# Optimization experiments

Measured on AMD Instinct MI355X. Metric: run time of the kernel, lower is better.

The kernel has to match this reference:

```python
import jax, jax.numpy as jnp
import numpy as np

C = 1024          # channels
H = 8             # num_channels (heads)
D = C // H        # channel_dim
POS = 16          # pos_dim (hard-coded in module)
MAX_FREQ = 16.0
MIN_FREQ = 1.0
HALF_S = 16       # samples_per_dim=32 -> offsets -16..16 -> S=33
S = 2 * HALF_S + 1


def setup_inputs() -> dict:
    key = jax.random.key(0)
    ks = jax.random.split(key, 8)
    B, L = 2, 2048
    s = 0.02  # realistic small init scale for learned weights
    return {
        "x": jax.random.normal(ks[0], (B, L, C), jnp.float32),
        "w_wave": jax.random.normal(ks[1], (3 * H, C), jnp.float32) * s,
        "b_wave": jnp.zeros((3 * H,), jnp.float32),
        "w_query": jax.random.normal(ks[2], (H * POS, C), jnp.float32) * s,
        "b_query": jnp.zeros((H * POS,), jnp.float32),
        "w_key": jax.random.normal(ks[3], (POS,), jnp.float32) * s,  # key_proj: Linear(1, POS, bias=False)
        "w_out": jax.random.normal(ks[4], (C, C), jnp.float32) * s,
        "w_se1": jax.random.normal(ks[5], (C // 4, C), jnp.float32) * s,
        "b_se1": jnp.zeros((C // 4,), jnp.float32),
        "w_se2": jax.random.normal(ks[6], (C, C // 4), jnp.float32) * s,
        "b_se2": jnp.zeros((C,), jnp.float32),
    }


def reference(x, w_wave, b_wave, w_query, b_query, w_key, w_out, w_se1, b_se1, w_se2, b_se2):
    B, L, Cc = x.shape
    offsets = jnp.arange(-HALF_S, HALF_S + 1, dtype=jnp.float32)  # stride_grid[:, 0], (S,)

    # wave params -> per-token, per-head freq / phase / decay
    wp = jax.nn.silu(x @ w_wave.T + b_wave).reshape(B, L, 3, H).transpose(0, 1, 3, 2)  # (B,L,H,3)
    freq = jax.nn.sigmoid(wp[..., 0]) * (MAX_FREQ - MIN_FREQ) + MIN_FREQ  # (B,L,H)
    phase = jnp.tanh(wp[..., 1]) * MAX_FREQ                               # (B,L,H)
    decay = jax.nn.sigmoid(wp[..., 2]) * 9.5 + 0.5                        # (B,L,H)
    freq_avg = freq.mean(axis=2)   # (B,L)
    phase_avg = phase.mean(axis=2) # (B,L)

    # learned fractional sample positions along the sequence
    centers = jnp.arange(L, dtype=jnp.float32)
    sample_pos = (centers[None, :, None]
                  + offsets[None, None, :] * freq_avg[..., None]
                  + phase_avg[..., None])                                 # (B,L,S)
    valid = (sample_pos >= 0) & (sample_pos < L)                          # (B,L,S)
    idx = jnp.clip(sample_pos.astype(jnp.int32), 0, L - 1)

    # dynamic gather of values at computed indices: (B,L,S,C)
    values = jax.vmap(lambda xf, i: xf[i])(x, idx)
    values = values.reshape(B, L, S, H, D).transpose(0, 1, 3, 2, 4)       # (B,L,H,S,D)

    queries = jax.nn.silu(x @ w_query.T + b_query).reshape(B, L, H, POS)  # (B,L,H,POS)
    rel_dist = jnp.abs(jnp.abs(offsets)[None, None, None, :] * freq[..., None])  # (B,L,H,S)
    keys = rel_dist[..., None] * w_key                                    # (B,L,H,S,POS)

    logits = jnp.einsum('blhd,blhsd->blhs', queries, keys) * (POS ** -0.5)
    vmask = valid[:, :, None, :]                                          # (B,L,1,S) -> broadcast (B,L,H,S)
    logits = jnp.where(vmask, logits, -jnp.inf)
    envelope = jnp.exp(-rel_dist / jnp.clip(decay[..., None], 0.1, None))

    attn = jax.nn.softmax(logits, axis=-1) * envelope * vmask
    attn = attn / (attn.sum(axis=-1, keepdims=True) + 1e-8)

    out = jnp.einsum('blhsd,blhs->blhd', values, attn).reshape(B, L, Cc)

    # SE-style channel gating
    se = jax.nn.sigmoid(jax.nn.silu(out @ w_se1.T + b_se1) @ w_se2.T + b_se2)
    out = (out * se) @ w_out.T                                            # (B,L,C) (spatial=(L,))

    entropy = -(attn * jnp.log(attn + 1e-8)).sum(axis=-1).mean()
    return out, -entropy
```

## Files before the change

kernel.cpp:

```cpp
#include <hip/hip_runtime.h>

typedef unsigned short u16;
typedef unsigned int u32;
typedef __attribute__((ext_vector_type(8))) __bf16 bf16x8;
typedef __attribute__((ext_vector_type(4))) float f32x4;

#define L_SEQ 2048
#define NROWS 4096
#define NHEAD 8
#define SWIN 33

__device__ __forceinline__ u16 f2b(float f) {
  u32 u = __float_as_uint(f);
  u += 0x7fffu + ((u >> 16) & 1u);
  return (u16)(u >> 16);
}
__device__ __forceinline__ float b2f(u32 lo16) { return __uint_as_float(lo16 << 16); }

__device__ __forceinline__ float sigmoidf_(float x) { return 1.f / (1.f + expf(-x)); }
__device__ __forceinline__ float siluf_(float x) { return x / (1.f + expf(-x)); }

__device__ __forceinline__ void gload_lds16(void* g, void* l) {
  __builtin_amdgcn_global_load_lds((__attribute__((address_space(1))) void*)g,
                                   (__attribute__((address_space(3))) void*)l, 16, 0, 0);
}

#define RPB 4
__global__ __launch_bounds__(256) void wave_params_kernel(
    const float* __restrict__ x, const float* __restrict__ w_wave,
    const float* __restrict__ b_wave, float* __restrict__ params,
    u16* __restrict__ xb,
    const float* __restrict__ wq, const float* __restrict__ w1,
    const float* __restrict__ w2, const float* __restrict__ wo,
    u16* __restrict__ wqb, u16* __restrict__ w1b, u16* __restrict__ w2b,
    u16* __restrict__ wob) {
  __shared__ float xs[RPB][1024];
  __shared__ float wp[RPB][24];
  const int t = threadIdx.x;
  const int bx = blockIdx.x;
  if (bx >= 1024) {
    size_t i = (size_t)(bx - 1024) * 256 + t;
    const float* src;
    u16* dst;
    if (i < 32768) { src = wq; dst = wqb; }
    else if ((i -= 32768) < 65536) { src = w1; dst = w1b; }
    else if ((i -= 65536) < 65536) { src = w2; dst = w2b; }
    else if ((i -= 65536) < 262144) { src = wo; dst = wob; }
    else return;
    const float4 v = *(const float4*)(src + i * 4);
    uint2 pk;
    pk.x = (u32)f2b(v.x) | ((u32)f2b(v.y) << 16);
    pk.y = (u32)f2b(v.z) | ((u32)f2b(v.w) << 16);
    *(uint2*)(dst + i * 4) = pk;
    return;
  }
  const int row0 = bx * RPB;
  const float4* xv = (const float4*)(x + (size_t)row0 * 1024);
  float4* xsv = (float4*)&xs[0][0];
  uint2* xbv = (uint2*)(xb + (size_t)row0 * 1024);
#pragma unroll
  for (int i = 0; i < RPB; ++i) {
    const float4 v = xv[t + 256 * i];
    xsv[t + 256 * i] = v;
    uint2 pk;
    pk.x = (u32)f2b(v.x) | ((u32)f2b(v.y) << 16);
    pk.y = (u32)f2b(v.z) | ((u32)f2b(v.w) << 16);
    xbv[t + 256 * i] = pk;
  }
  __syncthreads();
  const int wv = t >> 6, lane = t & 63;
#pragma unroll
  for (int oi = 0; oi < 6; ++oi) {
    const int o = wv * 6 + oi;
    float w[16];
#pragma unroll
    for (int k = 0; k < 16; ++k) w[k] = w_wave[o * 1024 + lane + 64 * k];
    const float bo = b_wave[o];
    float d[RPB];
#pragma unroll
    for (int r = 0; r < RPB; ++r) {
      d[r] = 0.f;
#pragma unroll
      for (int k = 0; k < 16; ++k) d[r] += w[k] * xs[r][lane + 64 * k];
    }
#pragma unroll
    for (int r = 0; r < RPB; ++r) {
#pragma unroll
      for (int off = 32; off; off >>= 1) d[r] += __shfl_xor(d[r], off);
    }
    if (lane == 0) {
#pragma unroll
      for (int r = 0; r < RPB; ++r) wp[r][o] = siluf_(d[r] + bo);
    }
  }
  __syncthreads();
  if (t < RPB * 8) {
    const int r = t >> 3, h = t & 7;
    float* pr = params + (size_t)(row0 + r) * 18;
    pr[h] = sigmoidf_(wp[r][h]) * 15.f + 1.f;
    pr[8 + h] = sigmoidf_(wp[r][16 + h]) * 9.5f + 0.5f;
  }
  if (t < RPB) {
    float fs = 0.f, ps = 0.f;
    for (int h = 0; h < 8; ++h) {
      fs += sigmoidf_(wp[t][h]);
      ps += tanhf(wp[t][8 + h]);
    }
    float* pr = params + (size_t)(row0 + t) * 18;
    pr[16] = fs * (15.f / 8.f) + 1.f;
    pr[17] = ps * (16.f / 8.f);
  }
}

template <int MODE, int TM, int TN, int BK, int ENT = 0>
__global__ __launch_bounds__(256) void gemm_bt(
    const u16* __restrict__ A, const u16* __restrict__ Bw,
    const float* __restrict__ bias, const u16* __restrict__ aux,
    const float* __restrict__ wkey, const float* __restrict__ entpart,
    float* __restrict__ entslot, void* __restrict__ outp, int N, int K) {
  __shared__ __align__(16) u16 As[2 * TM * BK];
  __shared__ __align__(16) u16 Bs[2 * TN * BK];
  const int t = threadIdx.x;
  const int bm = blockIdx.x, bn = blockIdx.y;
  if (ENT && bn == (int)gridDim.y - 1) {
    if (bm != 0) return;
    __shared__ float ws2[4];
    float s = 0.f;
#pragma unroll
    for (int i = 0; i < 16; ++i) s += entpart[t + 256 * i];
#pragma unroll
    for (int o = 32; o; o >>= 1) s += __shfl_xor(s, o);
    if ((t & 63) == 0) ws2[t >> 6] = s;
    __syncthreads();
    if (t == 0) *entslot = ws2[0] + ws2[1] + ws2[2] + ws2[3];
    return;
  }
  constexpr int TPR = BK / 8;
  constexpr int RPP = 256 / TPR;
  const int rowS = t / TPR;
  const int colX = ((t & (TPR - 1)) ^ (rowS & (TPR - 1))) * 8;
  const u16* Ag = A + (size_t)(bm * TM + rowS) * K + colX;
  const u16* Bg = Bw + (size_t)(bn * TN + rowS) * K + colX;
  constexpr int NI = TM / 32, NJ = TN / 32;
  f32x4 acc[NI][NJ] = {};
  const int lane = t & 63, wv = t >> 6;
  const int wm = (wv >> 1) * (TM / 2);
  const int wn = (wv & 1) * (TN / 2);
  const int frow = lane & 15, quad = lane >> 4;
  auto stage = [&](int buf, int kt) {
    char* Ab = (char*)As + buf * (TM * BK * 2);
    char* Bb = (char*)Bs + buf * (TN * BK * 2);
#pragma unroll
    for (int r = 0; r < TM; r += RPP)
      gload_lds16((void*)(Ag + kt + (size_t)r * K), Ab + r * BK * 2 + t * 16);
#pragma unroll
    for (int r = 0; r < TN; r += RPP)
      gload_lds16((void*)(Bg + kt + (size_t)r * K), Bb + r * BK * 2 + t * 16);
  };
  stage(0, 0);
  int pb = 0;
  for (int kt = 0; kt < K; kt += BK, pb ^= 1) {
    __syncthreads();
    if (kt + BK < K) stage(pb ^ 1, kt + BK);
#pragma unroll
    for (int kk = 0; kk < BK; kk += 32) {
      bf16x8 af[NI], bfr[NJ];
#pragma unroll
      for (int i = 0; i < NI; ++i) {
        const int rr = wm + i * 16 + frow;
        af[i] = *(bf16x8*)&As[pb * TM * BK + rr * BK + ((((kk >> 3) + quad) ^ (rr & (TPR - 1))) * 8)];
      }
#pragma unroll
      for (int j = 0; j < NJ; ++j) {
        const int rr = wn + j * 16 + frow;
        bfr[j] = *(bf16x8*)&Bs[pb * TN * BK + rr * BK + ((((kk >> 3) + quad) ^ (rr & (TPR - 1))) * 8)];
      }
#pragma unroll
      for (int i = 0; i < NI; ++i)
#pragma unroll
        for (int j = 0; j < NJ; ++j)
          acc[i][j] = __builtin_amdgcn_mfma_f32_16x16x32_bf16(af[i], bfr[j], acc[i][j], 0, 0, 0);
    }
  }
  if (MODE == 4) {
    const float bq = bias[bn * TN + wn + frow];
    const float wkf = wkey[frow];
    const int h = bn * 2 + (wn >> 4);
#pragma unroll
    for (int i = 0; i < NI; ++i)
#pragma unroll
      for (int r = 0; r < 4; ++r) {
        float w = siluf_(acc[i][0][r] + bq) * wkf;
        w += __shfl_xor(w, 1); w += __shfl_xor(w, 2);
        w += __shfl_xor(w, 4); w += __shfl_xor(w, 8);
        if (frow == 0) {
          const int gm = bm * TM + wm + i * 16 + quad * 4 + r;
          ((float*)outp)[gm * 8 + h] = w;
        }
      }
    return;
  }
#pragma unroll
  for (int i = 0; i < NI; ++i)
#pragma unroll
    for (int j = 0; j < NJ; ++j)
#pragma unroll
      for (int r = 0; r < 4; ++r) {
        const int gm = bm * TM + wm + i * 16 + quad * 4 + r;
        const int gn = bn * TN + wn + j * 16 + frow;
        float v = acc[i][j][r];
        const size_t o = (size_t)gm * N + gn;
        if (MODE == 0) { v = siluf_(v + bias[gn]); ((float*)outp)[o] = v; }
        if (MODE == 1) { v = siluf_(v + bias[gn]); ((u16*)outp)[o] = f2b(v); }
        if (MODE == 2) { v = sigmoidf_(v + bias[gn]) * b2f(aux[o]); ((u16*)outp)[o] = f2b(v); }
        if (MODE == 3) { ((float*)outp)[o] = v; }
      }
}

__global__ __launch_bounds__(256, 2) void attn_kernel(
    const u16* __restrict__ xb, const float* __restrict__ params,
    const float* __restrict__ qkbuf, u16* __restrict__ outb,
    float* __restrict__ entpart) {
  __shared__ float pf[18];
  __shared__ float qkL[8];
  __shared__ int idxL[SWIN];
  __shared__ int validL[SWIN];
  __shared__ float attnL[NHEAD][SWIN];
  __shared__ float entW[4];
  const int t = threadIdx.x;
  const int bx = blockIdx.x;
  const int row = ((bx & 7) << 9) | (bx >> 3);
  const int b = row >> 11, l = row & 2047;
  if (t < 18) pf[t] = params[(size_t)row * 18 + t];
  if (t >= 64 && t < 72) qkL[t - 64] = qkbuf[(size_t)row * 8 + (t - 64)] * 0.25f;
  __syncthreads();
  if (t < SWIN) {
    const float pos = (float)l + (float)(t - 16) * pf[16] + pf[17];
    validL[t] = (pos >= 0.f) && (pos < (float)L_SEQ);
    int id = (int)pos;
    idxL[t] = min(max(id, 0), L_SEQ - 1);
  }
  __syncthreads();
  const int wv = t >> 6, lane = t & 63;
  float entacc = 0.f;
#pragma unroll
  for (int it = 0; it < 2; ++it) {
    const int h = wv + 4 * it;
    const bool act = lane < SWIN;
    const int s = act ? lane : 0;
    const float rel = fabsf((float)(s - 16)) * pf[h];
    const float logit = rel * qkL[h];
    const bool vs = act && validL[s];
    float m = vs ? logit : -INFINITY;
#pragma unroll
    for (int o = 32; o; o >>= 1) m = fmaxf(m, __shfl_xor(m, o));
    float p = vs ? expf(logit - m) : 0.f;
    float sm = p;
#pragma unroll
    for (int o = 32; o; o >>= 1) sm += __shfl_xor(sm, o);
    const float soft = sm > 0.f ? p / sm : 0.f;
    const float env = expf(-rel / fmaxf(pf[8 + h], 0.1f));
    float a = soft * env;
    float as = a;
#pragma unroll
    for (int o = 32; o; o >>= 1) as += __shfl_xor(as, o);
    a = a / (as + 1e-8f);
    if (act) attnL[h][s] = a;
    float et = a * logf(a + 1e-8f);
#pragma unroll
    for (int o = 32; o; o >>= 1) et += __shfl_xor(et, o);
    entacc += et;
  }
  if (lane == 0) entW[wv] = entacc;
  __syncthreads();
  if (t == 0) entpart[bx] = (entW[0] + entW[1] + entW[2] + entW[3]) * (1.f / 32768.f);
  const u16* xbase = xb + (size_t)b * L_SEQ * 1024 + 4 * t;
  const int h = t >> 5;
  float4 acc = make_float4(0.f, 0.f, 0.f, 0.f);
  uint2 v0[17], v1[16];
#pragma unroll
  for (int k = 0; k < 17; ++k) v0[k] = *(const uint2*)(xbase + (size_t)idxL[k] * 1024);
  __builtin_amdgcn_sched_barrier(0);
#pragma unroll
  for (int k = 0; k < 16; ++k) v1[k] = *(const uint2*)(xbase + (size_t)idxL[17 + k] * 1024);
  __builtin_amdgcn_sched_barrier(0);
#pragma unroll
  for (int k = 0; k < 17; ++k) {
    const float a_ = attnL[h][k];
    acc.x += a_ * b2f(v0[k].x & 0xffffu);
    acc.y += a_ * b2f(v0[k].x >> 16);
    acc.z += a_ * b2f(v0[k].y & 0xffffu);
    acc.w += a_ * b2f(v0[k].y >> 16);
  }
  __builtin_amdgcn_sched_barrier(0);
#pragma unroll
  for (int k = 0; k < 16; ++k) {
    const float a_ = attnL[h][17 + k];
    acc.x += a_ * b2f(v1[k].x & 0xffffu);
    acc.y += a_ * b2f(v1[k].x >> 16);
    acc.z += a_ * b2f(v1[k].y & 0xffffu);
    acc.w += a_ * b2f(v1[k].y >> 16);
  }
  const size_t o4 = (size_t)row * 1024 + 4 * t;
  uint2 pk;
  pk.x = (u32)f2b(acc.x) | ((u32)f2b(acc.y) << 16);
  pk.y = (u32)f2b(acc.z) | ((u32)f2b(acc.w) << 16);
  *(uint2*)(outb + o4) = pk;
}

extern "C" void kernel_launch(void* const* d_in, const int* in_sizes, int n_in,
                              void* d_out, int out_size, void* d_ws, size_t ws_size,
                              hipStream_t stream) {
  const float* x = (const float*)d_in[0];
  const float* w_wave = (const float*)d_in[1];
  const float* b_wave = (const float*)d_in[2];
  const float* w_query = (const float*)d_in[3];
  const float* b_query = (const float*)d_in[4];
  const float* w_key = (const float*)d_in[5];
  const float* w_out = (const float*)d_in[6];
  const float* w_se1 = (const float*)d_in[7];
  const float* b_se1 = (const float*)d_in[8];
  const float* w_se2 = (const float*)d_in[9];
  const float* b_se2 = (const float*)d_in[10];
  float* out = (float*)d_out;
  char* ws = (char*)d_ws;
  size_t off = 0;
  auto alloc = [&](size_t bytes) { void* p = ws + off; off += (bytes + 255) & ~(size_t)255; return p; };
  float* params = (float*)alloc(NROWS * 18 * 4);
  float* qkbuf = (float*)alloc((size_t)NROWS * 8 * 4);
  float* entpart = (float*)alloc(NROWS * 4);
  u16* outb = (u16*)alloc((size_t)NROWS * 1024 * 2);
  u16* t1b = (u16*)alloc((size_t)NROWS * 256 * 2);
  u16* gb = (u16*)alloc((size_t)NROWS * 1024 * 2);
  u16* xb = (u16*)alloc((size_t)NROWS * 1024 * 2);
  u16* wqb = (u16*)alloc(128 * 1024 * 2);
  u16* w1b = (u16*)alloc(256 * 1024 * 2);
  u16* w2b = (u16*)alloc(1024 * 256 * 2);
  u16* wob = (u16*)alloc((size_t)1024 * 1024 * 2);
  float* entslot = out + (out_size - 1);

  wave_params_kernel<<<dim3(1024 + 1664), 256, 0, stream>>>(
      x, w_wave, b_wave, params, xb, w_query, w_se1, w_se2, w_out, wqb, w1b, w2b, wob);
  gemm_bt<4, 64, 32, 64><<<dim3(64, 4), 256, 0, stream>>>(
      xb, wqb, b_query, nullptr, w_key, nullptr, nullptr, qkbuf, 128, 1024);
  attn_kernel<<<dim3(NROWS), 256, 0, stream>>>(xb, params, qkbuf, outb, entpart);
  gemm_bt<1, 64, 32, 64, 1><<<dim3(64, 9), 256, 0, stream>>>(
      outb, w1b, b_se1, nullptr, nullptr, entpart, entslot, t1b, 256, 1024);
  gemm_bt<2, 128, 64, 64><<<dim3(32, 16), 256, 0, stream>>>(
      t1b, w2b, b_se2, outb, nullptr, nullptr, nullptr, gb, 1024, 256);
  gemm_bt<3, 128, 64, 64><<<dim3(32, 16), 256, 0, stream>>>(
      gb, wob, nullptr, nullptr, nullptr, nullptr, nullptr, out, 1024, 1024);
}
```

Before: 182.2 us.

## Fuse query projection GEMM into prologue kernel and enlarge SE/output GEMM tiles

The query-projection GEMM now runs inside the first kernel as 256 extra blocks. It reads fp32 x and w_query directly and converts them to bf16 in registers on the way into LDS. This removes one kernel launch and the separate w_query bf16 conversion, and lets that GEMM overlap with the wave-param and weight-conversion blocks. Separately, the SE1, SE2 and output GEMMs use wider N tiles (64 and 128), which halves their grid sizes and raises per-block reuse. The cost is fewer blocks to fill the CUs and more LDS per block in the fused kernel.

Result: slower. 188.9 us (+3.7%).

```diff
diff --git a/kernel.cpp b/kernel.cpp
--- a/kernel.cpp
+++ b/kernel.cpp
@@ -25,36 +25,108 @@
                                    (__attribute__((address_space(3))) void*)l, 16, 0, 0);
 }
 
+__device__ __forceinline__ uint2 pk2(float a, float b, float c, float d) {
+  uint2 p;
+  p.x = (u32)f2b(a) | ((u32)f2b(b) << 16);
+  p.y = (u32)f2b(c) | ((u32)f2b(d) << 16);
+  return p;
+}
+
 #define RPB 4
-__global__ __launch_bounds__(256) void wave_params_kernel(
+__global__ __launch_bounds__(256) void mega_kernel(
     const float* __restrict__ x, const float* __restrict__ w_wave,
     const float* __restrict__ b_wave, float* __restrict__ params,
     u16* __restrict__ xb,
-    const float* __restrict__ wq, const float* __restrict__ w1,
-    const float* __restrict__ w2, const float* __restrict__ wo,
-    u16* __restrict__ wqb, u16* __restrict__ w1b, u16* __restrict__ w2b,
-    u16* __restrict__ wob) {
+    const float* __restrict__ wq, const float* __restrict__ b_query,
+    const float* __restrict__ wkey, float* __restrict__ qkbuf,
+    const float* __restrict__ w1, const float* __restrict__ w2,
+    const float* __restrict__ wo,
+    u16* __restrict__ w1b, u16* __restrict__ w2b, u16* __restrict__ wob) {
   __shared__ float xs[RPB][1024];
   __shared__ float wp[RPB][24];
+  __shared__ __align__(16) u16 qkA[2][64 * 64];
+  __shared__ __align__(16) u16 qkB[2][32 * 64];
   const int t = threadIdx.x;
   const int bx = blockIdx.x;
-  if (bx >= 1024) {
-    size_t i = (size_t)(bx - 1024) * 256 + t;
+  const int lane = t & 63, wv = t >> 6;
+
+  if (bx < 256) {
+    const int bm = bx >> 2, bn = bx & 3;
+    const int rA = t >> 2, jA = t & 3;
+    const int rB = t >> 3, jB = t & 7;
+    const float* ag = x + (size_t)(bm * 64 + rA) * 1024 + 16 * jA;
+    const float* bg = wq + (size_t)(bn * 32 + rB) * 1024 + 8 * jB;
+    const int wm = (wv >> 1) * 32, wn = (wv & 1) * 16;
+    const int frow = lane & 15, quad = lane >> 4;
+    f32x4 acc[2] = {};
+    float4 a4[4], b4[2];
+    auto loadregs = [&](int kt) {
+#pragma unroll
+      for (int q = 0; q < 4; ++q) a4[q] = *(const float4*)(ag + kt + 4 * q);
+#pragma unroll
+      for (int q = 0; q < 2; ++q) b4[q] = *(const float4*)(bg + kt + 4 * q);
+    };
+    loadregs(0);
+    int pb = 0;
+    for (int kt = 0; kt < 1024; kt += 64, pb ^= 1) {
+      uint2 pa0 = pk2(a4[0].x, a4[0].y, a4[0].z, a4[0].w);
+      uint2 pa1 = pk2(a4[1].x, a4[1].y, a4[1].z, a4[1].w);
+      uint2 pa2 = pk2(a4[2].x, a4[2].y, a4[2].z, a4[2].w);
+      uint2 pa3 = pk2(a4[3].x, a4[3].y, a4[3].z, a4[3].w);
+      uint2 pb0 = pk2(b4[0].x, b4[0].y, b4[0].z, b4[0].w);
+      uint2 pb1 = pk2(b4[1].x, b4[1].y, b4[1].z, b4[1].w);
+      const int cA0 = (2 * jA) ^ (rA & 7), cA1 = (2 * jA + 1) ^ (rA & 7);
+      *(uint4*)&qkA[pb][rA * 64 + cA0 * 8] = make_uint4(pa0.x, pa0.y, pa1.x, pa1.y);
+      *(uint4*)&qkA[pb][rA * 64 + cA1 * 8] = make_uint4(pa2.x, pa2.y, pa3.x, pa3.y);
+      const int cB = jB ^ (rB & 7);
+      *(uint4*)&qkB[pb][rB * 64 + cB * 8] = make_uint4(pb0.x, pb0.y, pb1.x, pb1.y);
+      if (kt + 64 < 1024) loadregs(kt + 64);
+      __syncthreads();
+#pragma unroll
+      for (int kk = 0; kk < 64; kk += 32) {
+        bf16x8 af[2], bfr;
+#pragma unroll
+        for (int i = 0; i < 2; ++i) {
+          const int rr = wm + i * 16 + frow;
+          af[i] = *(bf16x8*)&qkA[pb][rr * 64 + ((((kk >> 3) + quad) ^ (rr & 7)) * 8)];
+        }
+        const int rn = wn + frow;
+        bfr = *(bf16x8*)&qkB[pb][rn * 64 + ((((kk >> 3) + quad) ^ (rn & 7)) * 8)];
+#pragma unroll
+        for (int i = 0; i < 2; ++i)
+          acc[i] = __builtin_amdgcn_mfma_f32_16x16x32_bf16(af[i], bfr, acc[i], 0, 0, 0);
+      }
+    }
+    const float bq = b_query[bn * 32 + wn + frow];
+    const float wkf = wkey[frow];
+    const int h = bn * 2 + (wv & 1);
+#pragma unroll
+    for (int i = 0; i < 2; ++i)
+#pragma unroll
+      for (int r = 0; r < 4; ++r) {
+        float w = siluf_(acc[i][r] + bq) * wkf;
+        w += __shfl_xor(w, 1); w += __shfl_xor(w, 2);
+        w += __shfl_xor(w, 4); w += __shfl_xor(w, 8);
+        if (frow == 0) {
+          const int gm = bm * 64 + wm + i * 16 + quad * 4 + r;
+          qkbuf[gm * 8 + h] = w;
+        }
+      }
+    return;
+  }
+  if (bx >= 1280) {
+    size_t i = (size_t)(bx - 1280) * 256 + t;
     const float* src;
     u16* dst;
-    if (i < 32768) { src = wq; dst = wqb; }
-    else if ((i -= 32768) < 65536) { src = w1; dst = w1b; }
+    if (i < 65536) { src = w1; dst = w1b; }
     else if ((i -= 65536) < 65536) { src = w2; dst = w2b; }
     else if ((i -= 65536) < 262144) { src = wo; dst = wob; }
     else return;
     const float4 v = *(const float4*)(src + i * 4);
-    uint2 pk;
-    pk.x = (u32)f2b(v.x) | ((u32)f2b(v.y) << 16);
-    pk.y = (u32)f2b(v.z) | ((u32)f2b(v.w) << 16);
-    *(uint2*)(dst + i * 4) = pk;
+    *(uint2*)(dst + i * 4) = pk2(v.x, v.y, v.z, v.w);
     return;
   }
-  const int row0 = bx * RPB;
+  const int row0 = (bx - 256) * RPB;
   const float4* xv = (const float4*)(x + (size_t)row0 * 1024);
   float4* xsv = (float4*)&xs[0][0];
   uint2* xbv = (uint2*)(xb + (size_t)row0 * 1024);
@@ -62,13 +134,9 @@
   for (int i = 0; i < RPB; ++i) {
     const float4 v = xv[t + 256 * i];
     xsv[t + 256 * i] = v;
-    uint2 pk;
-    pk.x = (u32)f2b(v.x) | ((u32)f2b(v.y) << 16);
-    pk.y = (u32)f2b(v.z) | ((u32)f2b(v.w) << 16);
-    xbv[t + 256 * i] = pk;
-  }
-  __syncthreads();
-  const int wv = t >> 6, lane = t & 63;
+    xbv[t + 256 * i] = pk2(v.x, v.y, v.z, v.w);
+  }
+  __syncthreads();
 #pragma unroll
   for (int oi = 0; oi < 6; ++oi) {
     const int o = wv * 6 + oi;
@@ -116,8 +184,8 @@
 __global__ __launch_bounds__(256) void gemm_bt(
     const u16* __restrict__ A, const u16* __restrict__ Bw,
     const float* __restrict__ bias, const u16* __restrict__ aux,
-    const float* __restrict__ wkey, const float* __restrict__ entpart,
-    float* __restrict__ entslot, void* __restrict__ outp, int N, int K) {
+    const float* __restrict__ entpart, float* __restrict__ entslot,
+    void* __restrict__ outp, int N, int K) {
   __shared__ __align__(16) u16 As[2 * TM * BK];
   __shared__ __align__(16) u16 Bs[2 * TN * BK];
   const int t = threadIdx.x;
@@ -182,24 +250,6 @@
           acc[i][j] = __builtin_amdgcn_mfma_f32_16x16x32_bf16(af[i], bfr[j], acc[i][j], 0, 0, 0);
     }
   }
-  if (MODE == 4) {
-    const float bq = bias[bn * TN + wn + frow];
-    const float wkf = wkey[frow];
-    const int h = bn * 2 + (wn >> 4);
-#pragma unroll
-    for (int i = 0; i < NI; ++i)
-#pragma unroll
-      for (int r = 0; r < 4; ++r) {
-        float w = siluf_(acc[i][0][r] + bq) * wkf;
-        w += __shfl_xor(w, 1); w += __shfl_xor(w, 2);
-        w += __shfl_xor(w, 4); w += __shfl_xor(w, 8);
-        if (frow == 0) {
-          const int gm = bm * TM + wm + i * 16 + quad * 4 + r;
-          ((float*)outp)[gm * 8 + h] = w;
-        }
-      }
-    return;
-  }
 #pragma unroll
   for (int i = 0; i < NI; ++i)
 #pragma unroll
@@ -210,7 +260,6 @@
         const int gn = bn * TN + wn + j * 16 + frow;
         float v = acc[i][j][r];
         const size_t o = (size_t)gm * N + gn;
-        if (MODE == 0) { v = siluf_(v + bias[gn]); ((float*)outp)[o] = v; }
         if (MODE == 1) { v = siluf_(v + bias[gn]); ((u16*)outp)[o] = f2b(v); }
         if (MODE == 2) { v = sigmoidf_(v + bias[gn]) * b2f(aux[o]); ((u16*)outp)[o] = f2b(v); }
         if (MODE == 3) { ((float*)outp)[o] = v; }
@@ -302,10 +351,7 @@
     acc.w += a_ * b2f(v1[k].y >> 16);
   }
   const size_t o4 = (size_t)row * 1024 + 4 * t;
-  uint2 pk;
-  pk.x = (u32)f2b(acc.x) | ((u32)f2b(acc.y) << 16);
-  pk.y = (u32)f2b(acc.z) | ((u32)f2b(acc.w) << 16);
-  *(uint2*)(outb + o4) = pk;
+  *(uint2*)(outb + o4) = pk2(acc.x, acc.y, acc.z, acc.w);
 }
 
 extern "C" void kernel_launch(void* const* d_in, const int* in_sizes, int n_in,
@@ -333,21 +379,19 @@
   u16* t1b = (u16*)alloc((size_t)NROWS * 256 * 2);
   u16* gb = (u16*)alloc((size_t)NROWS * 1024 * 2);
   u16* xb = (u16*)alloc((size_t)NROWS * 1024 * 2);
-  u16* wqb = (u16*)alloc(128 * 1024 * 2);
   u16* w1b = (u16*)alloc(256 * 1024 * 2);
   u16* w2b = (u16*)alloc(1024 * 256 * 2);
   u16* wob = (u16*)alloc((size_t)1024 * 1024 * 2);
   float* entslot = out + (out_size - 1);
 
-  wave_params_kernel<<<dim3(1024 + 1664), 256, 0, stream>>>(
-      x, w_wave, b_wave, params, xb, w_query, w_se1, w_se2, w_out, wqb, w1b, w2b, wob);
-  gemm_bt<4, 64, 32, 64><<<dim3(64, 4), 256, 0, stream>>>(
-      xb, wqb, b_query, nullptr, w_key, nullptr, nullptr, qkbuf, 128, 1024);
+  mega_kernel<<<dim3(2816), 256, 0, stream>>>(
+      x, w_wave, b_wave, params, xb, w_query, b_query, w_key, qkbuf,
+      w_se1, w_se2, w_out, w1b, w2b, wob);
   attn_kernel<<<dim3(NROWS), 256, 0, stream>>>(xb, params, qkbuf, outb, entpart);
-  gemm_bt<1, 64, 32, 64, 1><<<dim3(64, 9), 256, 0, stream>>>(
-      outb, w1b, b_se1, nullptr, nullptr, entpart, entslot, t1b, 256, 1024);
-  gemm_bt<2, 128, 64, 64><<<dim3(32, 16), 256, 0, stream>>>(
-      t1b, w2b, b_se2, outb, nullptr, nullptr, nullptr, gb, 1024, 256);
-  gemm_bt<3, 128, 64, 64><<<dim3(32, 16), 256, 0, stream>>>(
-      gb, wob, nullptr, nullptr, nullptr, nullptr, nullptr, out, 1024, 1024);
-}
+  gemm_bt<1, 64, 64, 64, 1><<<dim3(64, 5), 256, 0, stream>>>(
+      outb, w1b, b_se1, nullptr, entpart, entslot, t1b, 256, 1024);
+  gemm_bt<2, 128, 128, 64><<<dim3(32, 8), 256, 0, stream>>>(
+      t1b, w2b, b_se2, outb, nullptr, nullptr, gb, 1024, 256);
+  gemm_bt<3, 128, 128, 64><<<dim3(32, 8), 256, 0, stream>>>(
+      gb, wob, nullptr, nullptr, nullptr, nullptr, out, 1024, 1024);
+}
```
